# Performance work log

Measured on AMD Instinct MI355X. Metric: run time of the kernel, lower is better.

The kernel has to match this reference:

```python
import jax, jax.numpy as jnp
import numpy as np


def _filters(bmt):
    # bmt: (L,) low-pass h(-m1..m2). dec_lo = flip(h); g_tilde = flip(h)*(-1)^j;
    # dec_hi = flip(g_tilde)  (matches bmt_h / bmt_g_tilde / bmt_g in the torch code)
    L = bmt.shape[0]
    signs = 1.0 - 2.0 * (jnp.arange(L) % 2).astype(bmt.dtype)  # (+1,-1,+1,...)
    dec_lo = jnp.flip(bmt)
    g_tilde = dec_lo * signs
    dec_hi = jnp.flip(g_tilde)
    return dec_lo, dec_hi


def _conv_stride2(xp, w):
    # xp: (B,1,Npad), w: (L,) -> cross-correlation, stride 2, valid (== torch conv1d)
    return jax.lax.conv_general_dilated(xp, w[None, None, :], window_strides=(2,), padding='VALID')


def _dwt(x, dec_lo, dec_hi, m1, m2):
    # x: (B,K,N) -> (a, d) each (B,K,N//2). Periodic padding:
    # pad_periodic(x,n1,n2)[i] = x[(i-n1) mod N]  ==  jnp.pad mode='wrap'.
    B, K, N = x.shape
    xr = x.reshape(B * K, 1, N)
    xa = jnp.pad(xr, ((0, 0), (0, 0), (m1, m2)), mode='wrap')
    a = _conv_stride2(xa, dec_lo)
    xd = jnp.pad(xr, ((0, 0), (0, 0), (m2 - 1, m1 + 1)), mode='wrap')
    d = _conv_stride2(xd, dec_hi)
    return a.reshape(B, K, N // 2), d.reshape(B, K, N // 2)


def setup_inputs() -> dict:
    key = jax.random.key(0)
    k1, k2 = jax.random.split(key)
    x = jax.random.normal(k1, (32, 1024, 1024), dtype=jnp.float32)
    bmt = jax.random.normal(k2, (8,), dtype=jnp.float32)
    return {"x": x, "bmt": bmt, "m1": 3, "m2": 4}


def reference(x, bmt, m1, m2):
    # 2D fast wavelet transform in square format (Wav_2d_sqformat)
    dec_lo, dec_hi = _filters(bmt)
    cA, cD = _dwt(x, dec_lo, dec_hi, m1, m2)                       # rows filtered
    cAA, cAD = _dwt(cA.swapaxes(1, 2), dec_lo, dec_hi, m1, m2)     # cols of cA
    cDA, cDD = _dwt(cD.swapaxes(1, 2), dec_lo, dec_hi, m1, m2)     # cols of cD
    cAA, cAD = cAA.swapaxes(1, 2), cAD.swapaxes(1, 2)
    cDA, cDD = cDA.swapaxes(1, 2), cDD.swapaxes(1, 2)
    top = jnp.concatenate([cAA, cAD], axis=2)
    bot = jnp.concatenate([cDA, cDD], axis=2)
    return jnp.concatenate([top, bot], axis=1)  # (B,N,N)
```

## Files before the change

### kernel.cpp

```cpp
#include <hip/hip_runtime.h>

#define NN 1024
#define HH 512
#define TR 32
#define TC 32
#define S1R 70
#define XST 74
#define NF4 18
#define NLD ((S1R * NF4 + 255) / 256)
#define ADS 36

typedef float f2  __attribute__((ext_vector_type(2)));
typedef float f4v __attribute__((ext_vector_type(4)));

__device__ __forceinline__ void pk_fma_blo(f2& acc, f2 ab, f2 w) {
    asm("v_pk_fma_f32 %0, %1, %2, %0 op_sel:[0,0,0] op_sel_hi:[1,0,1]"
        : "+v"(acc) : "v"(ab), "v"(w));
}
__device__ __forceinline__ void pk_fma_bhi(f2& acc, f2 ab, f2 w) {
    asm("v_pk_fma_f32 %0, %1, %2, %0 op_sel:[0,1,0] op_sel_hi:[1,1,1]"
        : "+v"(acc) : "v"(ab), "v"(w));
}

__global__ __launch_bounds__(256, 4) void dwt2d_fused(const float* __restrict__ x,
                                                      const float* __restrict__ bmt,
                                                      float* __restrict__ out) {
    __shared__ float Xs[S1R][XST];
    __shared__ float As[S1R][ADS];
    __shared__ float Ds[S1R][ADS];

    const int tid = threadIdx.x;
    const int b  = blockIdx.z;
    const int R0 = blockIdx.y * TR;
    const int C0 = blockIdx.x * TC;

    f2 lohi[8];
#pragma unroll
    for (int j = 0; j < 8; ++j) {
        float l = bmt[7 - j];
        float v = bmt[j];
        f2 p; p.x = l; p.y = (j & 1) ? v : -v;
        lohi[j] = p;
    }

    const float* xb = x + (size_t)b * NN * NN;
    const int rbase = 2 * R0 - 3;
    const int pb    = 2 * C0 - 4;

    float4 v[NLD];
    int    su[NLD], st4[NLD];
#pragma unroll
    for (int k = 0; k < NLD; ++k) {
        int idx = tid + 256 * k;
        unsigned uu = (unsigned)idx / 18u;
        int tt = idx - 18 * (int)uu;
        su[k] = (int)uu; st4[k] = tt;
        int row = (rbase + (int)uu) & (NN - 1);
        int gc  = (pb + 4 * tt) & (NN - 1);
        v[k] = *(const float4*)(xb + ((size_t)row << 10) + gc);
    }
#pragma unroll
    for (int k = 0; k < NLD; ++k) {
        int idx = tid + 256 * k;
        if (idx < S1R * NF4) {
            int u = su[k];
            int q = 4 * st4[k] - 1;
            if (q >= 0) Xs[u][q] = v[k].x;
            f2 yz; yz.x = v[k].y; yz.y = v[k].z;
            *(f2*)&Xs[u][q + 1] = yz;
            Xs[u][q + 3] = v[k].w;
        }
    }
    __syncthreads();

    for (int pos = tid; pos < S1R * 8; pos += 256) {
        int u  = pos >> 3;
        int c0 = (pos & 7) * 4;
        const f2* wrow = (const f2*)&Xs[u][2 * c0];
        f2 w2[7];
#pragma unroll
        for (int t = 0; t < 7; ++t) w2[t] = wrow[t];
        f2 accs[4];
#pragma unroll
        for (int m = 0; m < 4; ++m) {
            f2 acc; acc.x = 0.f; acc.y = 0.f;
#pragma unroll
            for (int s = 0; s < 4; ++s) {
                pk_fma_blo(acc, lohi[2 * s],     w2[m + s]);
                pk_fma_bhi(acc, lohi[2 * s + 1], w2[m + s]);
            }
            accs[m] = acc;
        }
        f4v va, vd;
        va.x = accs[0].x; va.y = accs[1].x; va.z = accs[2].x; va.w = accs[3].x;
        vd.x = accs[0].y; vd.y = accs[1].y; vd.z = accs[2].y; vd.w = accs[3].y;
        *(f4v*)&As[u][c0] = va;
        *(f4v*)&Ds[u][c0] = vd;
    }
    __syncthreads();

    const int cg = tid & 7;
    const int r  = tid >> 3;
    f2 acc0[4], acc1[4];
#pragma unroll
    for (int i = 0; i < 4; ++i) {
        acc0[i].x = 0.f; acc0[i].y = 0.f;
        acc1[i].x = 0.f; acc1[i].y = 0.f;
    }
#pragma unroll
    for (int j = 0; j < 8; ++j) {
        f4v qa = *(const f4v*)&As[2 * r + j][4 * cg];
        f4v qd = *(const f4v*)&Ds[2 * r + j][4 * cg];
        f2 lh = lohi[j];
        f2 a01 = qa.xy, a23 = qa.zw, d01 = qd.xy, d23 = qd.zw;
        pk_fma_blo(acc0[0], lh, a01);
        pk_fma_bhi(acc0[1], lh, a01);
        pk_fma_blo(acc0[2], lh, a23);
        pk_fma_bhi(acc0[3], lh, a23);
        pk_fma_blo(acc1[0], lh, d01);
        pk_fma_bhi(acc1[1], lh, d01);
        pk_fma_blo(acc1[2], lh, d23);
        pk_fma_bhi(acc1[3], lh, d23);
    }
    float* ob = out + (size_t)b * NN * NN;
    const int orow = R0 + r;
    const int ocol = C0 + 4 * cg;
    *(float4*)(ob + (size_t)orow * NN + ocol)             = make_float4(acc0[0].x, acc0[1].x, acc0[2].x, acc0[3].x);
    *(float4*)(ob + (size_t)orow * NN + ocol + HH)        = make_float4(acc0[0].y, acc0[1].y, acc0[2].y, acc0[3].y);
    *(float4*)(ob + (size_t)(orow + HH) * NN + ocol)      = make_float4(acc1[0].x, acc1[1].x, acc1[2].x, acc1[3].x);
    *(float4*)(ob + (size_t)(orow + HH) * NN + ocol + HH) = make_float4(acc1[0].y, acc1[1].y, acc1[2].y, acc1[3].y);
}

extern "C" void kernel_launch(void* const* d_in, const int* in_sizes, int n_in,
                              void* d_out, int out_size, void* d_ws, size_t ws_size,
                              hipStream_t stream) {
    const float* x   = (const float*)d_in[0];
    const float* bmt = (const float*)d_in[1];
    float* out = (float*)d_out;
    const int B = in_sizes[0] / (NN * NN);
    dim3 grid(HH / TC, HH / TR, B);
    dwt2d_fused<<<grid, 256, 0, stream>>>(x, bmt, out);
}
```

Measured before the change: 231.2 us.

## Load input rows directly from global in row pass, drop shared staging tile

Removes the shared-memory input tile and its staging barrier. The row-filter stage now reads each thread's 16-float window straight from global memory with vector loads, relying on cache for the overlapping reads between neighbouring threads. This frees LDS, and the launch bound is raised to 8 blocks per CU to use the extra occupancy. The cost is redundant global/L2 traffic for the overlapping halo windows and possibly more register pressure under the tighter launch bound.

```diff
diff --git a/kernel.cpp b/kernel.cpp
--- a/kernel.cpp
+++ b/kernel.cpp
@@ -5,9 +5,6 @@
 #define TR 32
 #define TC 32
 #define S1R 70
-#define XST 74
-#define NF4 18
-#define NLD ((S1R * NF4 + 255) / 256)
 #define ADS 36
 
 typedef float f2  __attribute__((ext_vector_type(2)));
@@ -22,10 +19,9 @@
         : "+v"(acc) : "v"(ab), "v"(w));
 }
 
-__global__ __launch_bounds__(256, 4) void dwt2d_fused(const float* __restrict__ x,
+__global__ __launch_bounds__(256, 8) void dwt2d_fused(const float* __restrict__ x,
                                                       const float* __restrict__ bmt,
                                                       float* __restrict__ out) {
-    __shared__ float Xs[S1R][XST];
     __shared__ float As[S1R][ADS];
     __shared__ float Ds[S1R][ADS];
 
@@ -45,41 +41,22 @@
 
     const float* xb = x + (size_t)b * NN * NN;
     const int rbase = 2 * R0 - 3;
-    const int pb    = 2 * C0 - 4;
-
-    float4 v[NLD];
-    int    su[NLD], st4[NLD];
-#pragma unroll
-    for (int k = 0; k < NLD; ++k) {
-        int idx = tid + 256 * k;
-        unsigned uu = (unsigned)idx / 18u;
-        int tt = idx - 18 * (int)uu;
-        su[k] = (int)uu; st4[k] = tt;
-        int row = (rbase + (int)uu) & (NN - 1);
-        int gc  = (pb + 4 * tt) & (NN - 1);
-        v[k] = *(const float4*)(xb + ((size_t)row << 10) + gc);
-    }
-#pragma unroll
-    for (int k = 0; k < NLD; ++k) {
-        int idx = tid + 256 * k;
-        if (idx < S1R * NF4) {
-            int u = su[k];
-            int q = 4 * st4[k] - 1;
-            if (q >= 0) Xs[u][q] = v[k].x;
-            f2 yz; yz.x = v[k].y; yz.y = v[k].z;
-            *(f2*)&Xs[u][q + 1] = yz;
-            Xs[u][q + 3] = v[k].w;
-        }
-    }
-    __syncthreads();
 
     for (int pos = tid; pos < S1R * 8; pos += 256) {
         int u  = pos >> 3;
         int c0 = (pos & 7) * 4;
-        const f2* wrow = (const f2*)&Xs[u][2 * c0];
+        int ru = (rbase + u) & (NN - 1);
+        const float* xr = xb + ((size_t)ru << 10);
+        int bc = 2 * C0 + 2 * c0 - 4;
+        float f[16];
+#pragma unroll
+        for (int i = 0; i < 4; ++i) {
+            f4v t = *(const f4v*)(xr + ((bc + 4 * i) & (NN - 1)));
+            f[4 * i + 0] = t.x; f[4 * i + 1] = t.y; f[4 * i + 2] = t.z; f[4 * i + 3] = t.w;
+        }
         f2 w2[7];
 #pragma unroll
-        for (int t = 0; t < 7; ++t) w2[t] = wrow[t];
+        for (int t = 0; t < 7; ++t) { f2 p; p.x = f[2 * t + 1]; p.y = f[2 * t + 2]; w2[t] = p; }
         f2 accs[4];
 #pragma unroll
         for (int m = 0; m < 4; ++m) {
@@ -125,10 +102,14 @@
     float* ob = out + (size_t)b * NN * NN;
     const int orow = R0 + r;
     const int ocol = C0 + 4 * cg;
-    *(float4*)(ob + (size_t)orow * NN + ocol)             = make_float4(acc0[0].x, acc0[1].x, acc0[2].x, acc0[3].x);
-    *(float4*)(ob + (size_t)orow * NN + ocol + HH)        = make_float4(acc0[0].y, acc0[1].y, acc0[2].y, acc0[3].y);
-    *(float4*)(ob + (size_t)(orow + HH) * NN + ocol)      = make_float4(acc1[0].x, acc1[1].x, acc1[2].x, acc1[3].x);
-    *(float4*)(ob + (size_t)(orow + HH) * NN + ocol + HH) = make_float4(acc1[0].y, acc1[1].y, acc1[2].y, acc1[3].y);
+    f4v s0; s0.x = acc0[0].x; s0.y = acc0[1].x; s0.z = acc0[2].x; s0.w = acc0[3].x;
+    f4v s1; s1.x = acc0[0].y; s1.y = acc0[1].y; s1.z = acc0[2].y; s1.w = acc0[3].y;
+    f4v s2; s2.x = acc1[0].x; s2.y = acc1[1].x; s2.z = acc1[2].x; s2.w = acc1[3].x;
+    f4v s3; s3.x = acc1[0].y; s3.y = acc1[1].y; s3.z = acc1[2].y; s3.w = acc1[3].y;
+    *(f4v*)(ob + (size_t)orow * NN + ocol)             = s0;
+    *(f4v*)(ob + (size_t)orow * NN + ocol + HH)        = s1;
+    *(f4v*)(ob + (size_t)(orow + HH) * NN + ocol)      = s2;
+    *(f4v*)(ob + (size_t)(orow + HH) * NN + ocol + HH) = s3;
 }
 
 extern "C" void kernel_launch(void* const* d_in, const int* in_sizes, int n_in,
```

New measurement: 241.0 us. 4.2% more time.

## Process four row tiles per block with register-prefetched next input tile

Applied to the files above, without the earlier changes.

Each block now handles four consecutive 32-row output tiles instead of one, cutting the grid height by four. The global loads for the next tile's input rows are issued into registers before the current tile's row-filter pass and written to shared memory after it, so load latency overlaps compute. The change adds per-iteration barriers and extra registers for the prefetch buffer. It also reduces block-launch overhead and the lo/hi filter setup per tile, but there are fewer blocks for latency hiding and no halo reuse between tiles.

```diff
diff --git a/kernel.cpp b/kernel.cpp
--- a/kernel.cpp
+++ b/kernel.cpp
@@ -7,8 +7,9 @@
 #define S1R 70
 #define XST 74
 #define NF4 18
-#define NLD ((S1R * NF4 + 255) / 256)
+#define NLD 5
 #define ADS 36
+#define TILES 4
 
 typedef float f2  __attribute__((ext_vector_type(2)));
 typedef float f4v __attribute__((ext_vector_type(4)));
@@ -31,104 +32,145 @@
 
     const int tid = threadIdx.x;
     const int b  = blockIdx.z;
-    const int R0 = blockIdx.y * TR;
+    const int Rb = blockIdx.y * (TILES * TR);
     const int C0 = blockIdx.x * TC;
 
     f2 lohi[8];
 #pragma unroll
     for (int j = 0; j < 8; ++j) {
         float l = bmt[7 - j];
-        float v = bmt[j];
-        f2 p; p.x = l; p.y = (j & 1) ? v : -v;
+        float vv = bmt[j];
+        f2 p; p.x = l; p.y = (j & 1) ? vv : -vv;
         lohi[j] = p;
     }
 
     const float* xb = x + (size_t)b * NN * NN;
-    const int rbase = 2 * R0 - 3;
-    const int pb    = 2 * C0 - 4;
+    const int pb = 2 * C0 - 4;
 
-    float4 v[NLD];
-    int    su[NLD], st4[NLD];
+    int su[NLD], gcol[NLD], qq[NLD];
+    bool wr[NLD];
 #pragma unroll
     for (int k = 0; k < NLD; ++k) {
         int idx = tid + 256 * k;
         unsigned uu = (unsigned)idx / 18u;
         int tt = idx - 18 * (int)uu;
-        su[k] = (int)uu; st4[k] = tt;
-        int row = (rbase + (int)uu) & (NN - 1);
-        int gc  = (pb + 4 * tt) & (NN - 1);
-        v[k] = *(const float4*)(xb + ((size_t)row << 10) + gc);
+        su[k]   = (int)uu;
+        gcol[k] = (pb + 4 * tt) & (NN - 1);
+        qq[k]   = 4 * tt - 1;
+        wr[k]   = idx < S1R * NF4;
     }
+
+    {
+        const int rbase = 2 * Rb - 3;
+        float4 v[NLD];
 #pragma unroll
-    for (int k = 0; k < NLD; ++k) {
-        int idx = tid + 256 * k;
-        if (idx < S1R * NF4) {
-            int u = su[k];
-            int q = 4 * st4[k] - 1;
-            if (q >= 0) Xs[u][q] = v[k].x;
-            f2 yz; yz.x = v[k].y; yz.y = v[k].z;
-            *(f2*)&Xs[u][q + 1] = yz;
-            Xs[u][q + 3] = v[k].w;
+        for (int k = 0; k < NLD; ++k) {
+            int row = (rbase + su[k]) & (NN - 1);
+            v[k] = *(const float4*)(xb + ((size_t)row << 10) + gcol[k]);
+        }
+#pragma unroll
+        for (int k = 0; k < NLD; ++k) {
+            if (wr[k]) {
+                int u = su[k], q = qq[k];
+                if (q >= 0) Xs[u][q] = v[k].x;
+                f2 yz; yz.x = v[k].y; yz.y = v[k].z;
+                *(f2*)&Xs[u][q + 1] = yz;
+                Xs[u][q + 3] = v[k].w;
+            }
         }
     }
     __syncthreads();
 
-    for (int pos = tid; pos < S1R * 8; pos += 256) {
-        int u  = pos >> 3;
-        int c0 = (pos & 7) * 4;
-        const f2* wrow = (const f2*)&Xs[u][2 * c0];
-        f2 w2[7];
+#pragma unroll 1
+    for (int t = 0; t < TILES; ++t) {
+        const int R0 = Rb + t * TR;
+
+        float4 vn[NLD];
+        if (t < TILES - 1) {
+            const int rbase = 2 * (R0 + TR) - 3;
 #pragma unroll
-        for (int t = 0; t < 7; ++t) w2[t] = wrow[t];
-        f2 accs[4];
+            for (int k = 0; k < NLD; ++k) {
+                int row = (rbase + su[k]) & (NN - 1);
+                vn[k] = *(const float4*)(xb + ((size_t)row << 10) + gcol[k]);
+            }
+        }
+
+        for (int pos = tid; pos < S1R * 8; pos += 256) {
+            int u  = pos >> 3;
+            int c0 = (pos & 7) * 4;
+            const f2* wrow = (const f2*)&Xs[u][2 * c0];
+            f2 w2[7];
 #pragma unroll
-        for (int m = 0; m < 4; ++m) {
-            f2 acc; acc.x = 0.f; acc.y = 0.f;
+            for (int q = 0; q < 7; ++q) w2[q] = wrow[q];
+            f2 accs[4];
 #pragma unroll
-            for (int s = 0; s < 4; ++s) {
-                pk_fma_blo(acc, lohi[2 * s],     w2[m + s]);
-                pk_fma_bhi(acc, lohi[2 * s + 1], w2[m + s]);
+            for (int m = 0; m < 4; ++m) {
+                f2 acc; acc.x = 0.f; acc.y = 0.f;
+#pragma unroll
+                for (int s = 0; s < 4; ++s) {
+                    pk_fma_blo(acc, lohi[2 * s],     w2[m + s]);
+                    pk_fma_bhi(acc, lohi[2 * s + 1], w2[m + s]);
+                }
+                accs[m] = acc;
             }
-            accs[m] = acc;
+            f4v va, vd;
+            va.x = accs[0].x; va.y = accs[1].x; va.z = accs[2].x; va.w = accs[3].x;
+            vd.x = accs[0].y; vd.y = accs[1].y; vd.z = accs[2].y; vd.w = accs[3].y;
+            *(f4v*)&As[u][c0] = va;
+            *(f4v*)&Ds[u][c0] = vd;
         }
-        f4v va, vd;
-        va.x = accs[0].x; va.y = accs[1].x; va.z = accs[2].x; va.w = accs[3].x;
-        vd.x = accs[0].y; vd.y = accs[1].y; vd.z = accs[2].y; vd.w = accs[3].y;
-        *(f4v*)&As[u][c0] = va;
-        *(f4v*)&Ds[u][c0] = vd;
+        __syncthreads();
+
+        if (t < TILES - 1) {
+#pragma unroll
+            for (int k = 0; k < NLD; ++k) {
+                if (wr[k]) {
+                    int u = su[k], q = qq[k];
+                    if (q >= 0) Xs[u][q] = vn[k].x;
+                    f2 yz; yz.x = vn[k].y; yz.y = vn[k].z;
+                    *(f2*)&Xs[u][q + 1] = yz;
+                    Xs[u][q + 3] = vn[k].w;
+                }
+            }
+        }
+
+        const int cg = tid & 7;
+        const int r  = tid >> 3;
+        f2 acc0[4], acc1[4];
+#pragma unroll
+        for (int i = 0; i < 4; ++i) {
+            acc0[i].x = 0.f; acc0[i].y = 0.f;
+            acc1[i].x = 0.f; acc1[i].y = 0.f;
+        }
+#pragma unroll
+        for (int j = 0; j < 8; ++j) {
+            f4v qa = *(const f4v*)&As[2 * r + j][4 * cg];
+            f4v qd = *(const f4v*)&Ds[2 * r + j][4 * cg];
+            f2 lh = lohi[j];
+            f2 a01 = qa.xy, a23 = qa.zw, d01 = qd.xy, d23 = qd.zw;
+            pk_fma_blo(acc0[0], lh, a01);
+            pk_fma_bhi(acc0[1], lh, a01);
+            pk_fma_blo(acc0[2], lh, a23);
+            pk_fma_bhi(acc0[3], lh, a23);
+            pk_fma_blo(acc1[0], lh, d01);
+            pk_fma_bhi(acc1[1], lh, d01);
+            pk_fma_blo(acc1[2], lh, d23);
+            pk_fma_bhi(acc1[3], lh, d23);
+        }
+        float* ob = out + (size_t)b * NN * NN;
+        const int orow = R0 + r;
+        const int ocol = C0 + 4 * cg;
+        f4v s0; s0.x = acc0[0].x; s0.y = acc0[1].x; s0.z = acc0[2].x; s0.w = acc0[3].x;
+        f4v s1; s1.x = acc0[0].y; s1.y = acc0[1].y; s1.z = acc0[2].y; s1.w = acc0[3].y;
+        f4v s2; s2.x = acc1[0].x; s2.y = acc1[1].x; s2.z = acc1[2].x; s2.w = acc1[3].x;
+        f4v s3; s3.x = acc1[0].y; s3.y = acc1[1].y; s3.z = acc1[2].y; s3.w = acc1[3].y;
+        *(f4v*)(ob + (size_t)orow * NN + ocol)             = s0;
+        *(f4v*)(ob + (size_t)orow * NN + ocol + HH)        = s1;
+        *(f4v*)(ob + (size_t)(orow + HH) * NN + ocol)      = s2;
+        *(f4v*)(ob + (size_t)(orow + HH) * NN + ocol + HH) = s3;
+
+        __syncthreads();
     }
-    __syncthreads();
-
-    const int cg = tid & 7;
-    const int r  = tid >> 3;
-    f2 acc0[4], acc1[4];
-#pragma unroll
-    for (int i = 0; i < 4; ++i) {
-        acc0[i].x = 0.f; acc0[i].y = 0.f;
-        acc1[i].x = 0.f; acc1[i].y = 0.f;
-    }
-#pragma unroll
-    for (int j = 0; j < 8; ++j) {
-        f4v qa = *(const f4v*)&As[2 * r + j][4 * cg];
-        f4v qd = *(const f4v*)&Ds[2 * r + j][4 * cg];
-        f2 lh = lohi[j];
-        f2 a01 = qa.xy, a23 = qa.zw, d01 = qd.xy, d23 = qd.zw;
-        pk_fma_blo(acc0[0], lh, a01);
-        pk_fma_bhi(acc0[1], lh, a01);
-        pk_fma_blo(acc0[2], lh, a23);
-        pk_fma_bhi(acc0[3], lh, a23);
-        pk_fma_blo(acc1[0], lh, d01);
-        pk_fma_bhi(acc1[1], lh, d01);
-        pk_fma_blo(acc1[2], lh, d23);
-        pk_fma_bhi(acc1[3], lh, d23);
-    }
-    float* ob = out + (size_t)b * NN * NN;
-    const int orow = R0 + r;
-    const int ocol = C0 + 4 * cg;
-    *(float4*)(ob + (size_t)orow * NN + ocol)             = make_float4(acc0[0].x, acc0[1].x, acc0[2].x, acc0[3].x);
-    *(float4*)(ob + (size_t)orow * NN + ocol + HH)        = make_float4(acc0[0].y, acc0[1].y, acc0[2].y, acc0[3].y);
-    *(float4*)(ob + (size_t)(orow + HH) * NN + ocol)      = make_float4(acc1[0].x, acc1[1].x, acc1[2].x, acc1[3].x);
-    *(float4*)(ob + (size_t)(orow + HH) * NN + ocol + HH) = make_float4(acc1[0].y, acc1[1].y, acc1[2].y, acc1[3].y);
 }
 
 extern "C" void kernel_launch(void* const* d_in, const int* in_sizes, int n_in,
@@ -138,6 +180,6 @@
     const float* bmt = (const float*)d_in[1];
     float* out = (float*)d_out;
     const int B = in_sizes[0] / (NN * NN);
-    dim3 grid(HH / TC, HH / TR, B);
+    dim3 grid(HH / TC, HH / (TR * TILES), B);
     dwt2d_fused<<<grid, 256, 0, stream>>>(x, bmt, out);
 }
```

New measurement: 241.4 us. +4.4%, slower.

## Fuse row and column filtering in registers, dropping intermediate shared buffers

Applied to the files above, without the earlier changes.

Removes the As/Ds shared-memory stage and the second barrier. Each thread now recomputes the row-filter outputs it needs directly from the input tile for every vertical tap, then accumulates the column filter in registers. This cuts LDS usage, allowing higher occupancy (launch bounds raised to 7 blocks), and the Xs stride is changed to avoid bank conflicts. The cost is redundant row-filter arithmetic, roughly four times more FMAs, since overlapping rows are recomputed.

```diff
diff --git a/kernel.cpp b/kernel.cpp
--- a/kernel.cpp
+++ b/kernel.cpp
@@ -5,10 +5,9 @@
 #define TR 32
 #define TC 32
 #define S1R 70
-#define XST 74
+#define XST 82
 #define NF4 18
-#define NLD ((S1R * NF4 + 255) / 256)
-#define ADS 36
+#define NLD 5
 
 typedef float f2  __attribute__((ext_vector_type(2)));
 typedef float f4v __attribute__((ext_vector_type(4)));
@@ -22,12 +21,10 @@
         : "+v"(acc) : "v"(ab), "v"(w));
 }
 
-__global__ __launch_bounds__(256, 4) void dwt2d_fused(const float* __restrict__ x,
+__global__ __launch_bounds__(256, 7) void dwt2d_fused(const float* __restrict__ x,
                                                       const float* __restrict__ bmt,
                                                       float* __restrict__ out) {
     __shared__ float Xs[S1R][XST];
-    __shared__ float As[S1R][ADS];
-    __shared__ float Ds[S1R][ADS];
 
     const int tid = threadIdx.x;
     const int b  = blockIdx.z;
@@ -38,8 +35,8 @@
 #pragma unroll
     for (int j = 0; j < 8; ++j) {
         float l = bmt[7 - j];
-        float v = bmt[j];
-        f2 p; p.x = l; p.y = (j & 1) ? v : -v;
+        float vv = bmt[j];
+        f2 p; p.x = l; p.y = (j & 1) ? vv : -vv;
         lohi[j] = p;
     }
 
@@ -73,32 +70,6 @@
     }
     __syncthreads();
 
-    for (int pos = tid; pos < S1R * 8; pos += 256) {
-        int u  = pos >> 3;
-        int c0 = (pos & 7) * 4;
-        const f2* wrow = (const f2*)&Xs[u][2 * c0];
-        f2 w2[7];
-#pragma unroll
-        for (int t = 0; t < 7; ++t) w2[t] = wrow[t];
-        f2 accs[4];
-#pragma unroll
-        for (int m = 0; m < 4; ++m) {
-            f2 acc; acc.x = 0.f; acc.y = 0.f;
-#pragma unroll
-            for (int s = 0; s < 4; ++s) {
-                pk_fma_blo(acc, lohi[2 * s],     w2[m + s]);
-                pk_fma_bhi(acc, lohi[2 * s + 1], w2[m + s]);
-            }
-            accs[m] = acc;
-        }
-        f4v va, vd;
-        va.x = accs[0].x; va.y = accs[1].x; va.z = accs[2].x; va.w = accs[3].x;
-        vd.x = accs[0].y; vd.y = accs[1].y; vd.z = accs[2].y; vd.w = accs[3].y;
-        *(f4v*)&As[u][c0] = va;
-        *(f4v*)&Ds[u][c0] = vd;
-    }
-    __syncthreads();
-
     const int cg = tid & 7;
     const int r  = tid >> 3;
     f2 acc0[4], acc1[4];
@@ -109,26 +80,34 @@
     }
 #pragma unroll
     for (int j = 0; j < 8; ++j) {
-        f4v qa = *(const f4v*)&As[2 * r + j][4 * cg];
-        f4v qd = *(const f4v*)&Ds[2 * r + j][4 * cg];
+        const f2* wrow = (const f2*)&Xs[2 * r + j][8 * cg];
+        f2 w2[7];
+#pragma unroll
+        for (int t = 0; t < 7; ++t) w2[t] = wrow[t];
         f2 lh = lohi[j];
-        f2 a01 = qa.xy, a23 = qa.zw, d01 = qd.xy, d23 = qd.zw;
-        pk_fma_blo(acc0[0], lh, a01);
-        pk_fma_bhi(acc0[1], lh, a01);
-        pk_fma_blo(acc0[2], lh, a23);
-        pk_fma_bhi(acc0[3], lh, a23);
-        pk_fma_blo(acc1[0], lh, d01);
-        pk_fma_bhi(acc1[1], lh, d01);
-        pk_fma_blo(acc1[2], lh, d23);
-        pk_fma_bhi(acc1[3], lh, d23);
+#pragma unroll
+        for (int m = 0; m < 4; ++m) {
+            f2 ad; ad.x = 0.f; ad.y = 0.f;
+#pragma unroll
+            for (int s = 0; s < 4; ++s) {
+                pk_fma_blo(ad, lohi[2 * s],     w2[m + s]);
+                pk_fma_bhi(ad, lohi[2 * s + 1], w2[m + s]);
+            }
+            pk_fma_blo(acc0[m], lh, ad);
+            pk_fma_bhi(acc1[m], lh, ad);
+        }
     }
     float* ob = out + (size_t)b * NN * NN;
     const int orow = R0 + r;
     const int ocol = C0 + 4 * cg;
-    *(float4*)(ob + (size_t)orow * NN + ocol)             = make_float4(acc0[0].x, acc0[1].x, acc0[2].x, acc0[3].x);
-    *(float4*)(ob + (size_t)orow * NN + ocol + HH)        = make_float4(acc0[0].y, acc0[1].y, acc0[2].y, acc0[3].y);
-    *(float4*)(ob + (size_t)(orow + HH) * NN + ocol)      = make_float4(acc1[0].x, acc1[1].x, acc1[2].x, acc1[3].x);
-    *(float4*)(ob + (size_t)(orow + HH) * NN + ocol + HH) = make_float4(acc1[0].y, acc1[1].y, acc1[2].y, acc1[3].y);
+    f4v s0; s0.x = acc0[0].x; s0.y = acc0[1].x; s0.z = acc0[2].x; s0.w = acc0[3].x;
+    f4v s1; s1.x = acc0[0].y; s1.y = acc0[1].y; s1.z = acc0[2].y; s1.w = acc0[3].y;
+    f4v s2; s2.x = acc1[0].x; s2.y = acc1[1].x; s2.z = acc1[2].x; s2.w = acc1[3].x;
+    f4v s3; s3.x = acc1[0].y; s3.y = acc1[1].y; s3.z = acc1[2].y; s3.w = acc1[3].y;
+    *(f4v*)(ob + (size_t)orow * NN + ocol)             = s0;
+    *(f4v*)(ob + (size_t)orow * NN + ocol + HH)        = s1;
+    *(f4v*)(ob + (size_t)(orow + HH) * NN + ocol)      = s2;
+    *(f4v*)(ob + (size_t)(orow + HH) * NN + ocol + HH) = s3;
 }
 
 extern "C" void kernel_launch(void* const* d_in, const int* in_sizes, int n_in,
```

New measurement: 234.9 us. About the same (+1.6%).
